# Kernel tuning notes

Measured on AMD Instinct MI355X. Metric: run time of the kernel, lower is better.

Reference implementation:

```python
import jax, jax.numpy as jnp
import numpy as np

B, S, D = 4, 1024, 2048
H, KVH, HD = 32, 8, 64
N_REP = H // KVH  # 4
ROPE_THETA = 1000000.0


def _rope_tables(seq_len, head_dim, theta):
    inv_freq = 1.0 / (theta ** (np.arange(0, head_dim, 2, dtype=np.float32) / head_dim))
    t = np.arange(seq_len, dtype=np.float32)
    freqs = np.outer(t, inv_freq)                      # (S, HD/2)
    emb = np.concatenate([freqs, freqs], axis=-1)      # (S, HD)
    return jnp.asarray(np.cos(emb)), jnp.asarray(np.sin(emb))


def setup_inputs() -> dict:
    key = jax.random.key(0)
    kx, kq, kk, kv, ko = jax.random.split(key, 5)
    cos, sin = _rope_tables(S, HD, ROPE_THETA)
    s = 0.02
    return {
        "x": jax.random.normal(kx, (B, S, D), jnp.float32),
        "cos": cos,
        "sin": sin,
        "Wq": jax.random.normal(kq, (D, H * HD), jnp.float32) * s,
        "Wk": jax.random.normal(kk, (D, KVH * HD), jnp.float32) * s,
        "Wv": jax.random.normal(kv, (D, KVH * HD), jnp.float32) * s,
        "Wo": jax.random.normal(ko, (H * HD, D), jnp.float32) * s,
    }


def _rotate_half(t):
    t1, t2 = jnp.split(t, 2, axis=-1)
    return jnp.concatenate([-t2, t1], axis=-1)


def reference(x, cos, sin, Wq, Wk, Wv, Wo):
    # projections
    q = (x @ Wq).reshape(B, S, H, HD)      # (b, s, h, d)
    k = (x @ Wk).reshape(B, S, KVH, HD)
    v = (x @ Wv).reshape(B, S, KVH, HD)

    # RoPE: cos/sin (s, d) broadcast over heads (unsqueeze_dim=1 -> (s,1,d))
    c = cos[:, None, :]
    sn = sin[:, None, :]
    q = q * c + _rotate_half(q) * sn
    k = k * c + _rotate_half(k) * sn

    # GQA attention without physically repeating KV:
    # q grouped as (b, kvh, n_rep, s, d); repeat_kv '(h r)' maps q head g*n_rep+r -> kv head g
    qg = q.transpose(0, 2, 1, 3).reshape(B, KVH, N_REP, S, HD)
    kt = k.transpose(0, 2, 1, 3)  # (b, kvh, s, d)
    vt = v.transpose(0, 2, 1, 3)

    scale = 1.0 / jnp.sqrt(jnp.asarray(HD, x.dtype))
    scores = jnp.einsum('bgrqd,bgkd->bgrqk', qg, kt) * scale  # (b, kvh, rep, s, s)
    probs = jax.nn.softmax(scores, axis=-1)
    out = jnp.einsum('bgrqk,bgkd->bgrqd', probs, vt)           # (b, kvh, rep, s, d)

    out = out.reshape(B, H, S, HD).transpose(0, 2, 1, 3).reshape(B, S, H * HD)
    return out @ Wo
```

## Files before the change

### kernel.cpp

```cpp
#include <hip/hip_runtime.h>

typedef unsigned short u16;
typedef __attribute__((ext_vector_type(8))) __bf16 bf16x8;
typedef __attribute__((ext_vector_type(4))) _Float16 f16x4;
typedef __attribute__((ext_vector_type(8))) _Float16 f16x8;
typedef __attribute__((ext_vector_type(4))) float f32x4;

#define BB 4
#define SS 1024
#define DD 2048
#define HH 32
#define KVHN 8
#define HDIM 64

__device__ __forceinline__ u16 f2b(float f) {
    union { float f; unsigned u; } v; v.f = f;
    unsigned r = v.u + 0x7FFFu + ((v.u >> 16) & 1u);
    return (u16)(r >> 16);
}
__device__ __forceinline__ float b2f(u16 h) {
    union { unsigned u; float f; } v; v.u = ((unsigned)h) << 16; return v.f;
}

__device__ __forceinline__ f32x4 mfma16(bf16x8 a, bf16x8 b, f32x4 c) {
    return __builtin_amdgcn_mfma_f32_16x16x32_bf16(a, b, c, 0, 0, 0);
}
__device__ __forceinline__ f32x4 mfma16h(f16x8 a, f16x8 b, f32x4 c) {
    return __builtin_amdgcn_mfma_f32_16x16x32_f16(a, b, c, 0, 0, 0);
}

__device__ __forceinline__ void async_cp16(const void* g, void* l) {
    __builtin_amdgcn_global_load_lds((__attribute__((address_space(1))) void*)g,
                                     (__attribute__((address_space(3))) void*)l,
                                     16, 0, 0);
}

__device__ __forceinline__ void block_sync() {
    asm volatile("" ::: "memory");
    __builtin_amdgcn_s_barrier();
    asm volatile("" ::: "memory");
}

__device__ __forceinline__ f16x8 pack8_f16(const float* p) {
    union { unsigned u[4]; f16x8 v; } pu;
    pu.u[0] = __builtin_bit_cast(unsigned, __builtin_amdgcn_cvt_pkrtz(p[0], p[1]));
    pu.u[1] = __builtin_bit_cast(unsigned, __builtin_amdgcn_cvt_pkrtz(p[2], p[3]));
    pu.u[2] = __builtin_bit_cast(unsigned, __builtin_amdgcn_cvt_pkrtz(p[4], p[5]));
    pu.u[3] = __builtin_bit_cast(unsigned, __builtin_amdgcn_cvt_pkrtz(p[6], p[7]));
    return pu.v;
}

__global__ __launch_bounds__(256) void cast_x_kernel(const float* __restrict__ x,
                                                     u16* __restrict__ xb) {
    int i = (blockIdx.x * 256 + threadIdx.x) * 4;
    float4 v = *(const float4*)(x + i);
    unsigned r0 = (unsigned)f2b(v.x) | ((unsigned)f2b(v.y) << 16);
    unsigned r1 = (unsigned)f2b(v.z) | ((unsigned)f2b(v.w) << 16);
    *(uint2*)(xb + i) = make_uint2(r0, r1);
}

__global__ __launch_bounds__(256) void wtrans_all_kernel(const float* __restrict__ Wq,
                                                         const float* __restrict__ Wk,
                                                         const float* __restrict__ Wv,
                                                         const float* __restrict__ Wo,
                                                         u16* __restrict__ Wqkvt,
                                                         u16* __restrict__ Wot) {
    __shared__ float tile[32][33];
    int z = blockIdx.z;
    const float* W = (z == 0) ? Wq : (z == 1) ? Wk : (z == 2) ? Wv : Wo;
    int N = (z == 1 || z == 2) ? 512 : 2048;
    int n_off = (z == 1) ? 2048 : (z == 2) ? 2560 : 0;
    u16* Wt = (z == 3) ? Wot : Wqkvt;
    int n0 = blockIdx.x * 32;
    if (n0 >= N) return;
    int k0 = blockIdx.y * 32;
    int tid = threadIdx.x;
    int nj = tid & 31;
    int ki = tid >> 5;
#pragma unroll
    for (int it = 0; it < 4; it++) {
        int kk = it * 8 + ki;
        tile[kk][nj] = W[(size_t)(k0 + kk) * N + n0 + nj];
    }
    __syncthreads();
#pragma unroll
    for (int it = 0; it < 4; it++) {
        int nn = it * 8 + ki;
        Wt[(size_t)(n0 + nn + n_off) * 2048 + k0 + nj] = f2b(tile[nj][nn]);
    }
}

__global__ __launch_bounds__(512, 2) void gemm_qkv(const u16* __restrict__ A,
                                                   const u16* __restrict__ Bt,
                                                   u16* __restrict__ C) {
    __shared__ __align__(16) u16 Ls[2][32768];
    const int tid = threadIdx.x;
    const int lane = tid & 63;
    const int w = tid >> 6;

    const int bid = blockIdx.x;
    const int xcd = bid & 7;
    const int loc = bid >> 3;
    const int mt = (xcd & 3) * 4 + (loc & 3);
    const int nt = (xcd >> 2) * 6 + (loc >> 2);
    const int m0 = mt * 256;
    const int n0 = nt * 256;

    const int wm = (w >> 2) * 128;
    const int wn = (w & 3) * 64;
    const int lr = lane & 15;
    const int lg = lane >> 4;

    const int row0 = tid >> 2;
    const int g = tid & 3;
    const int sg = g ^ ((row0 >> 1) & 3);
    const u16* pA0 = A + (size_t)(m0 + row0) * 2048 + sg * 8;
    const u16* pA1 = pA0 + (size_t)128 * 2048;
    const u16* pB0 = Bt + (size_t)(n0 + row0) * 2048 + sg * 8;
    const u16* pB1 = pB0 + (size_t)128 * 2048;

#define QSTA(buf_, ks_, T_)                                                     \
    {                                                                           \
        async_cp16(pA0 + (T_) * 64 + (ks_) * 32, &Ls[buf_][(ks_) * 8192 + w * 512]);        \
        async_cp16(pA1 + (T_) * 64 + (ks_) * 32, &Ls[buf_][(ks_) * 8192 + 4096 + w * 512]); \
    }
#define QSTB(buf_, ks_, T_)                                                     \
    {                                                                           \
        async_cp16(pB0 + (T_) * 64 + (ks_) * 32, &Ls[buf_][16384 + (ks_) * 8192 + w * 512]);        \
        async_cp16(pB1 + (T_) * 64 + (ks_) * 32, &Ls[buf_][16384 + (ks_) * 8192 + 4096 + w * 512]); \
    }

    f32x4 acc[8][4];
    const f32x4 zero4 = {0.f, 0.f, 0.f, 0.f};
#pragma unroll
    for (int i = 0; i < 8; i++)
#pragma unroll
        for (int j = 0; j < 4; j++) acc[i][j] = zero4;

    bf16x8 af[8], bfr[4];

#define QLDA(ks_)                                                               \
    _Pragma("unroll") for (int mi = 0; mi < 8; mi++) {                          \
        int r_ = wm + mi * 16 + lr;                                             \
        af[mi] = *(const bf16x8*)(&Ls[cur][(ks_) * 8192 + r_ * 32 + ((lg ^ ((r_ >> 1) & 3)) * 8)]); \
    }
#define QLDB(ks_, nb_)                                                          \
    _Pragma("unroll") for (int q_ = 0; q_ < 2; q_++) {                          \
        int ni_ = (nb_) * 2 + q_;                                               \
        int r_ = wn + ni_ * 16 + lr;                                            \
        bfr[ni_] = *(const bf16x8*)(&Ls[cur][16384 + (ks_) * 8192 + r_ * 32 + ((lg ^ ((r_ >> 1) & 3)) * 8)]); \
    }
#define QMM(nb_)                                                                \
    __builtin_amdgcn_s_setprio(1);                                              \
    _Pragma("unroll") for (int mi = 0; mi < 8; mi++) _Pragma("unroll") for (int q_ = 0; q_ < 2; q_++) { \
        int ni_ = (nb_) * 2 + q_;                                               \
        acc[mi][ni_] = mfma16(af[mi], bfr[ni_], acc[mi][ni_]);                  \
    }                                                                           \
    __builtin_amdgcn_s_setprio(0);
#define QWAITMM                                                                 \
    asm volatile("s_waitcnt lgkmcnt(0)" ::: "memory");                          \
    __builtin_amdgcn_sched_barrier(0);

    QSTA(0, 0, 0); QSTB(0, 0, 0); QSTA(0, 1, 0); QSTB(0, 1, 0);
    QSTA(1, 0, 1); QSTB(1, 0, 1);
    asm volatile("s_waitcnt vmcnt(4)" ::: "memory");
    block_sync();

#pragma unroll 2
    for (int T = 0; T < 32; ++T) {
        const int cur = T & 1;
        const int oth = cur ^ 1;
        const int Tp1 = (T + 1) & 31;
        const int Tp2 = (T + 2) & 31;

        QLDA(0); QLDB(0, 0);
        QSTA(oth, 1, Tp1);
        block_sync(); QWAITMM;
        QMM(0);
        block_sync();
        QLDB(0, 1);
        QSTB(oth, 1, Tp1);
        block_sync(); QWAITMM;
        QMM(1);
        block_sync();
        QLDA(1); QLDB(1, 0);
        QSTA(cur, 0, Tp2);
        block_sync(); QWAITMM;
        QMM(0);
        block_sync();
        QLDB(1, 1);
        QSTB(cur, 0, Tp2);
        block_sync(); QWAITMM;
        QMM(1);
        asm volatile("s_waitcnt vmcnt(4)" ::: "memory");
        block_sync();
    }
    asm volatile("s_waitcnt vmcnt(0)" ::: "memory");

    const int lq = lg * 4;
#pragma unroll
    for (int mi = 0; mi < 8; mi++)
#pragma unroll
        for (int ni = 0; ni < 4; ni++)
#pragma unroll
            for (int i = 0; i < 4; i++) {
                int r = m0 + wm + mi * 16 + lq + i;
                int c = n0 + wn + ni * 16 + lr;
                C[(size_t)r * 3072 + c] = f2b(acc[mi][ni][i]);
            }
#undef QSTA
#undef QSTB
#undef QLDA
#undef QLDB
#undef QMM
#undef QWAITMM
}

__global__ __launch_bounds__(512, 2) void gemm_out(const u16* __restrict__ A,
                                                   const u16* __restrict__ Bt,
                                                   float* __restrict__ C) {
    __shared__ __align__(16) u16 Ls[2][24576];
    const int tid = threadIdx.x;
    const int lane = tid & 63;
    const int w = tid >> 6;

    const int bid = blockIdx.x;
    const int xcd = bid & 7;
    const int loc = bid >> 3;
    const int mt = (xcd & 3) * 4 + (loc & 3);
    const int nt = (xcd >> 2) * 8 + (loc >> 2);
    const int m0 = mt * 256;
    const int n0 = nt * 128;

    const int wm = (w >> 2) * 128;
    const int wn = (w & 3) * 32;
    const int lr = lane & 15;
    const int lg = lane >> 4;

    const int row0 = tid >> 2;
    const int g = tid & 3;
    const int sg = g ^ ((row0 >> 1) & 3);
    const u16* pA0 = A + (size_t)(m0 + row0) * 2048 + sg * 8;
    const u16* pA1 = pA0 + (size_t)128 * 2048;
    const u16* pB0 = Bt + (size_t)(n0 + row0) * 2048 + sg * 8;

#define OSTA(buf_, ks_, T_)                                                     \
    {                                                                           \
        async_cp16(pA0 + (T_) * 64 + (ks_) * 32, &Ls[buf_][(ks_) * 8192 + w * 512]);        \
        async_cp16(pA1 + (T_) * 64 + (ks_) * 32, &Ls[buf_][(ks_) * 8192 + 4096 + w * 512]); \
    }
#define OSTB(buf_, ks_, T_)                                                     \
    {                                                                           \
        async_cp16(pB0 + (T_) * 64 + (ks_) * 32, &Ls[buf_][16384 + (ks_) * 4096 + w * 512]); \
    }

    f32x4 acc[8][2];
    const f32x4 zero4 = {0.f, 0.f, 0.f, 0.f};
#pragma unroll
    for (int i = 0; i < 8; i++)
#pragma unroll
        for (int j = 0; j < 2; j++) acc[i][j] = zero4;

    bf16x8 af[8], bfr[2];

#define OLDA(ks_)                                                               \
    _Pragma("unroll") for (int mi = 0; mi < 8; mi++) {                          \
        int r_ = wm + mi * 16 + lr;                                             \
        af[mi] = *(const bf16x8*)(&Ls[cur][(ks_) * 8192 + r_ * 32 + ((lg ^ ((r_ >> 1) & 3)) * 8)]); \
    }
#define OLDB(ks_)                                                               \
    _Pragma("unroll") for (int ni = 0; ni < 2; ni++) {                          \
        int r_ = wn + ni * 16 + lr;                                             \
        bfr[ni] = *(const bf16x8*)(&Ls[cur][16384 + (ks_) * 4096 + r_ * 32 + ((lg ^ ((r_ >> 1) & 3)) * 8)]); \
    }
#define OMM                                                                     \
    __builtin_amdgcn_s_setprio(1);                                              \
    _Pragma("unroll") for (int mi = 0; mi < 8; mi++) _Pragma("unroll") for (int ni = 0; ni < 2; ni++) { \
        acc[mi][ni] = mfma16(af[mi], bfr[ni], acc[mi][ni]);                     \
    }                                                                           \
    __builtin_amdgcn_s_setprio(0);
#define OWAITMM                                                                 \
    asm volatile("s_waitcnt lgkmcnt(0)" ::: "memory");                          \
    __builtin_amdgcn_sched_barrier(0);

    OSTA(0, 0, 0); OSTB(0, 0, 0); OSTA(0, 1, 0); OSTB(0, 1, 0);
    OSTA(1, 0, 1); OSTB(1, 0, 1);
    asm volatile("s_waitcnt vmcnt(3)" ::: "memory");
    block_sync();

#pragma unroll 2
    for (int T = 0; T < 32; ++T) {
        const int cur = T & 1;
        const int oth = cur ^ 1;
        const int Tp1 = (T + 1) & 31;
        const int Tp2 = (T + 2) & 31;

        OLDA(0); OLDB(0);
        OSTA(oth, 1, Tp1); OSTB(oth, 1, Tp1);
        block_sync(); OWAITMM;
        OMM;
        block_sync();
        OLDA(1); OLDB(1);
        OSTA(cur, 0, Tp2); OSTB(cur, 0, Tp2);
        block_sync(); OWAITMM;
        OMM;
        asm volatile("s_waitcnt vmcnt(3)" ::: "memory");
        block_sync();
    }
    asm volatile("s_waitcnt vmcnt(0)" ::: "memory");

    const int lq = lg * 4;
#pragma unroll
    for (int mi = 0; mi < 8; mi++)
#pragma unroll
        for (int ni = 0; ni < 2; ni++)
#pragma unroll
            for (int i = 0; i < 4; i++) {
                int r = m0 + wm + mi * 16 + lq + i;
                int c = n0 + wn + ni * 16 + lr;
                C[(size_t)r * 2048 + c] = acc[mi][ni][i];
            }
#undef OSTA
#undef OSTB
#undef OLDA
#undef OLDB
#undef OMM
#undef OWAITMM
}

__global__ __launch_bounds__(256) void rope_kernel(const u16* __restrict__ QKV,
                                                   const float* __restrict__ cosT,
                                                   const float* __restrict__ sinT,
                                                   u16* __restrict__ Qh,
                                                   u16* __restrict__ Kh) {
    const float QSC = 0.125f * 1.44269504088896f;
    int idx = blockIdx.x * 256 + threadIdx.x;
    int d = idx & 31;
    int t = idx >> 5;
    int hh = t % 40;
    int row = t / 40;
    int s = row & (SS - 1);
    int b = row >> 10;
    float c = cosT[s * HDIM + d];
    float sn = sinT[s * HDIM + d];
    if (hh < 32) {
        const u16* src = QKV + (size_t)row * 3072 + hh * 64 + d;
        float x1 = b2f(src[0]), x2 = b2f(src[32]);
        u16* dst = Qh + ((size_t)(b * HH + hh) * SS + s) * 64 + d;
        dst[0] = f2b((x1 * c - x2 * sn) * QSC);
        dst[32] = f2b((x2 * c + x1 * sn) * QSC);
    } else {
        int g = hh - 32;
        const u16* src = QKV + (size_t)row * 3072 + 2048 + g * 64 + d;
        float x1 = b2f(src[0]), x2 = b2f(src[32]);
        int rr = s & 7;
        int kpos = (s & ~31) + ((rr >= 4) ? 16 : 0) + ((s >> 3) & 3) * 4 + (rr & 3);
        u16* dst = Kh + ((size_t)(b * KVHN + g) * SS + kpos) * 64 + d;
        dst[0] = f2b(x1 * c - x2 * sn);
        dst[32] = f2b(x2 * c + x1 * sn);
    }
}

__global__ __launch_bounds__(256) void vtrans_kernel(const u16* __restrict__ QKV,
                                                     u16* __restrict__ Vt) {
    __shared__ u16 tile[64][65];
    int blk = blockIdx.x;
    int st = blk & 15;
    int t2 = blk >> 4;
    int g = t2 & 7;
    int b = t2 >> 3;
    int tid = threadIdx.x;
    int cj = tid & 63;
    int ri = tid >> 6;
    const u16* src = QKV + ((size_t)(b * SS + st * 64)) * 3072 + 2560 + g * 64;
#pragma unroll
    for (int it = 0; it < 16; it++) {
        int s_i = it * 4 + ri;
        tile[s_i][cj] = src[(size_t)s_i * 3072 + cj];
    }
    __syncthreads();
    u16* dst = Vt + ((size_t)(b * KVHN + g) * HDIM) * SS + st * 64;
#pragma unroll
    for (int it = 0; it < 16; it++) {
        int hd_i = it * 4 + ri;
        _Float16 hv = (_Float16)b2f(tile[cj][hd_i]);
        union { _Float16 h; u16 u; } cv; cv.h = hv;
        dst[(size_t)hd_i * SS + cj] = cv.u;
    }
}

__global__ __launch_bounds__(256, 4) void flash_kernel(const u16* __restrict__ Qh,
                                                       const u16* __restrict__ Kh,
                                                       const u16* __restrict__ Vt,
                                                       u16* __restrict__ Attn) {
    __shared__ __align__(16) u16 Kls[2][4096];
    __shared__ __align__(16) u16 Vls[2][4096];
    const int tid = threadIdx.x;
    const int lane = tid & 63;
    const int w = tid >> 6;
    const int bid = blockIdx.x;
    const int gbp = ((bid & 7) << 2) | ((bid >> 3) & 3);
    const int qt = bid >> 5;
    const int g = gbp & 7;
    const int b = gbp >> 3;
    const int h = g * 4 + w;
    const int lr = lane & 15;
    const int lg = lane >> 4;
    const int lk8 = lg * 8;
    const int lq = lg * 4;

    const u16* Qbase = Qh + ((size_t)(b * HH + h) * SS + qt * 32) * HDIM;
    bf16x8 qb[2][2];
#pragma unroll
    for (int j = 0; j < 2; j++) {
        qb[j][0] = *(const bf16x8*)(Qbase + (size_t)(j * 16 + lr) * HDIM + lk8);
        qb[j][1] = *(const bf16x8*)(Qbase + (size_t)(j * 16 + lr) * HDIM + 32 + lk8);
    }

    const u16* Kbase = Kh + (size_t)(b * KVHN + g) * SS * HDIM;
    const u16* Vbase = Vt + (size_t)(b * KVHN + g) * HDIM * SS;

    const int r0 = tid >> 3;
    const int c0 = tid & 7;

    const f32x4 zero4 = {0.f, 0.f, 0.f, 0.f};
    const f32x4 initS = {-4.f, -4.f, -4.f, -4.f};
    f32x4 o[2][4];
    float lsum[2] = {0.f, 0.f};
#pragma unroll
    for (int j = 0; j < 2; j++)
#pragma unroll
        for (int i = 0; i < 4; i++) o[j][i] = zero4;

#define STAGE(kt, p)                                                              \
    {                                                                             \
        _Pragma("unroll") for (int sh = 0; sh < 2; sh++) {                        \
            int rr = r0 + sh * 32;                                                \
            int cs = c0 ^ (rr & 7);                                              \
            async_cp16(Kbase + (size_t)((kt) + rr) * HDIM + cs * 8,               \
                       &Kls[p][sh * 2048 + w * 512]);                             \
            async_cp16(Vbase + (size_t)rr * SS + (kt) + cs * 8,                   \
                       &Vls[p][sh * 2048 + w * 512]);                             \
        }                                                                         \
    }

    STAGE(0, 0);
    __syncthreads();

    for (int t = 0; t < 16; t++) {
        const int p = t & 1;
        if (t < 15) STAGE((t + 1) * 64, p ^ 1);

#pragma unroll
        for (int c = 0; c < 2; c++) {
            f32x4 s[2][2];
#pragma unroll
            for (int halfi = 0; halfi < 2; halfi++) {
                const int R = c * 32 + halfi * 16 + lr;
                const u16* kr = &Kls[p][R * 64];
                bf16x8 kb0 = *(const bf16x8*)(kr + ((lg ^ (R & 7)) * 8));
                bf16x8 kb1 = *(const bf16x8*)(kr + (((4 + lg) ^ (R & 7)) * 8));
#pragma unroll
                for (int j = 0; j < 2; j++) {
                    f32x4 a = initS;
                    a = mfma16(kb0, qb[j][0], a);
                    a = mfma16(kb1, qb[j][1], a);
                    s[halfi][j] = a;
                }
            }

            f16x8 va[4];
#pragma unroll
            for (int hdt = 0; hdt < 4; hdt++) {
                const int R2 = hdt * 16 + lr;
                va[hdt] = *(const f16x8*)(&Vls[p][R2 * 64 + (((c * 4 + lg) ^ (R2 & 7)) * 8)]);
            }

#pragma unroll
            for (int j = 0; j < 2; j++) {
                float pv[8];
#pragma unroll
                for (int r = 0; r < 4; r++) {
                    pv[r] = __builtin_amdgcn_exp2f(s[0][j][r]);
                    pv[4 + r] = __builtin_amdgcn_exp2f(s[1][j][r]);
                }
                lsum[j] += ((pv[0] + pv[1]) + (pv[2] + pv[3])) +
                           ((pv[4] + pv[5]) + (pv[6] + pv[7]));
                f16x8 pb = pack8_f16(pv);
#pragma unroll
                for (int hdt = 0; hdt < 4; hdt++)
                    o[j][hdt] = mfma16h(va[hdt], pb, o[j][hdt]);
            }
        }
        __syncthreads();
    }

#pragma unroll
    for (int j = 0; j < 2; j++) {
        float su = lsum[j];
        su += __shfl_xor(su, 16);
        su += __shfl_xor(su, 32);
        float inv = 1.f / su;
        u16* Ob = Attn + ((size_t)(b * SS + qt * 32 + j * 16 + lr)) * 2048 + h * 64;
#pragma unroll
        for (int hdt = 0; hdt < 4; hdt++) {
            unsigned r0p = (unsigned)f2b(o[j][hdt][0] * inv) | ((unsigned)f2b(o[j][hdt][1] * inv) << 16);
            unsigned r1p = (unsigned)f2b(o[j][hdt][2] * inv) | ((unsigned)f2b(o[j][hdt][3] * inv) << 16);
            *(uint2*)(Ob + hdt * 16 + lq) = make_uint2(r0p, r1p);
        }
    }
}

extern "C" void kernel_launch(void* const* d_in, const int* in_sizes, int n_in,
                              void* d_out, int out_size, void* d_ws, size_t ws_size,
                              hipStream_t stream) {
    (void)in_sizes; (void)n_in; (void)out_size; (void)ws_size;
    const float* x = (const float*)d_in[0];
    const float* cosT = (const float*)d_in[1];
    const float* sinT = (const float*)d_in[2];
    const float* Wq = (const float*)d_in[3];
    const float* Wk = (const float*)d_in[4];
    const float* Wv = (const float*)d_in[5];
    const float* Wo = (const float*)d_in[6];
    float* out = (float*)d_out;

    char* ws = (char*)d_ws;
    u16* Xb    = (u16*)(ws);
    u16* Wqkvt = (u16*)(ws + 16777216);
    u16* Wot   = (u16*)(ws + 29360128);
    u16* QKV   = (u16*)(ws + 37748736);
    u16* Qh    = (u16*)(ws + 62914560);
    u16* Kh    = (u16*)(ws + 79691776);
    u16* Vt    = (u16*)(ws + 83886080);
    u16* Attn  = (u16*)(ws + 88080384);

    cast_x_kernel<<<8192, 256, 0, stream>>>(x, Xb);
    wtrans_all_kernel<<<dim3(64, 64, 4), 256, 0, stream>>>(Wq, Wk, Wv, Wo, Wqkvt, Wot);

    gemm_qkv<<<192, 512, 0, stream>>>(Xb, Wqkvt, QKV);

    rope_kernel<<<20480, 256, 0, stream>>>(QKV, cosT, sinT, Qh, Kh);
    vtrans_kernel<<<512, 256, 0, stream>>>(QKV, Vt);

    flash_kernel<<<1024, 256, 0, stream>>>(Qh, Kh, Vt, Attn);

    gemm_out<<<256, 512, 0, stream>>>(Attn, Wot, out);
}
```

Before: 270.5 us.

## Restructure QKV GEMM shared-memory layout and ping-pong load schedule

Rewrites the QKV projection GEMM's staging so each row holds a full 64-wide K slice with an 8-way XOR swizzle. The main loop now splits the 256x256 tile into M/N halves that are loaded and multiplied in a staggered order, with A and B tiles refilled into alternate buffers. The intent is to improve overlap of async global-to-LDS copies with MFMA work and to cut LDS bank conflicts and per-iteration barriers. The staggered buffer reuse makes the correctness of the wait counts and barrier placement delicate.

Measured after the change: 272.2 us. About the same (+0.6%).

```diff
diff --git a/kernel.cpp b/kernel.cpp
--- a/kernel.cpp
+++ b/kernel.cpp
@@ -106,28 +106,25 @@
     const int m0 = mt * 256;
     const int n0 = nt * 256;
 
-    const int wm = (w >> 2) * 128;
+    const int wm_h = w >> 2;
     const int wn = (w & 3) * 64;
     const int lr = lane & 15;
     const int lg = lane >> 4;
 
-    const int row0 = tid >> 2;
-    const int g = tid & 3;
-    const int sg = g ^ ((row0 >> 1) & 3);
-    const u16* pA0 = A + (size_t)(m0 + row0) * 2048 + sg * 8;
-    const u16* pA1 = pA0 + (size_t)128 * 2048;
-    const u16* pB0 = Bt + (size_t)(n0 + row0) * 2048 + sg * 8;
-    const u16* pB1 = pB0 + (size_t)128 * 2048;
-
-#define QSTA(buf_, ks_, T_)                                                     \
-    {                                                                           \
-        async_cp16(pA0 + (T_) * 64 + (ks_) * 32, &Ls[buf_][(ks_) * 8192 + w * 512]);        \
-        async_cp16(pA1 + (T_) * 64 + (ks_) * 32, &Ls[buf_][(ks_) * 8192 + 4096 + w * 512]); \
-    }
-#define QSTB(buf_, ks_, T_)                                                     \
-    {                                                                           \
-        async_cp16(pB0 + (T_) * 64 + (ks_) * 32, &Ls[buf_][16384 + (ks_) * 8192 + w * 512]);        \
-        async_cp16(pB1 + (T_) * 64 + (ks_) * 32, &Ls[buf_][16384 + (ks_) * 8192 + 4096 + w * 512]); \
+    const int sr = lane >> 3;
+    const int sl = (lane & 7) ^ (sr & 7);
+    const u16* pA = A + (size_t)(m0 + w * 8 + sr) * 2048 + sl * 8;
+    const u16* pB = Bt + (size_t)(n0 + w * 8 + sr) * 2048 + sl * 8;
+
+#define STA(buf_, h_, kt_)                                                               \
+    {                                                                                    \
+        async_cp16(pA + (size_t)((h_) * 128) * 2048 + (kt_) * 64, &Ls[buf_][(h_) * 8192 + w * 512]);            \
+        async_cp16(pA + (size_t)((h_) * 128 + 64) * 2048 + (kt_) * 64, &Ls[buf_][(h_) * 8192 + 4096 + w * 512]); \
+    }
+#define STB(buf_, h_, kt_)                                                               \
+    {                                                                                    \
+        async_cp16(pB + (size_t)((h_) * 128) * 2048 + (kt_) * 64, &Ls[buf_][16384 + (h_) * 8192 + w * 512]);            \
+        async_cp16(pB + (size_t)((h_) * 128 + 64) * 2048 + (kt_) * 64, &Ls[buf_][16384 + (h_) * 8192 + 4096 + w * 512]); \
     }
 
     f32x4 acc[8][4];
@@ -137,67 +134,86 @@
 #pragma unroll
         for (int j = 0; j < 4; j++) acc[i][j] = zero4;
 
-    bf16x8 af[8], bfr[4];
-
-#define QLDA(ks_)                                                               \
-    _Pragma("unroll") for (int mi = 0; mi < 8; mi++) {                          \
-        int r_ = wm + mi * 16 + lr;                                             \
-        af[mi] = *(const bf16x8*)(&Ls[cur][(ks_) * 8192 + r_ * 32 + ((lg ^ ((r_ >> 1) & 3)) * 8)]); \
-    }
-#define QLDB(ks_, nb_)                                                          \
-    _Pragma("unroll") for (int q_ = 0; q_ < 2; q_++) {                          \
-        int ni_ = (nb_) * 2 + q_;                                               \
-        int r_ = wn + ni_ * 16 + lr;                                            \
-        bfr[ni_] = *(const bf16x8*)(&Ls[cur][16384 + (ks_) * 8192 + r_ * 32 + ((lg ^ ((r_ >> 1) & 3)) * 8)]); \
-    }
-#define QMM(nb_)                                                                \
-    __builtin_amdgcn_s_setprio(1);                                              \
-    _Pragma("unroll") for (int mi = 0; mi < 8; mi++) _Pragma("unroll") for (int q_ = 0; q_ < 2; q_++) { \
-        int ni_ = (nb_) * 2 + q_;                                               \
-        acc[mi][ni_] = mfma16(af[mi], bfr[ni_], acc[mi][ni_]);                  \
-    }                                                                           \
+    bf16x8 af[8], b0[4], b1[4];
+
+#define LDA(mh_, buf_)                                                                   \
+    _Pragma("unroll") for (int mi = 0; mi < 4; mi++) _Pragma("unroll") for (int ks = 0; ks < 2; ks++) { \
+        int rh = (mh_) * 64 + mi * 16 + lr;                                              \
+        af[mi * 2 + ks] = *(const bf16x8*)(&Ls[buf_][wm_h * 8192 + rh * 64 + (((ks * 4 + lg) ^ (lr & 7)) * 8)]); \
+    }
+#define LDB(dst_, nh_, buf_)                                                             \
+    _Pragma("unroll") for (int ni = 0; ni < 2; ni++) _Pragma("unroll") for (int ks = 0; ks < 2; ks++) { \
+        int rowb = wn + (nh_) * 32 + ni * 16 + lr;                                       \
+        dst_[ni * 2 + ks] = *(const bf16x8*)(&Ls[buf_][16384 + (rowb >> 7) * 8192 + (rowb & 127) * 64 + (((ks * 4 + lg) ^ (lr & 7)) * 8)]); \
+    }
+#define QMM(mh_, nh_, bb_)                                                               \
+    __builtin_amdgcn_s_setprio(1);                                                       \
+    _Pragma("unroll") for (int mi = 0; mi < 4; mi++) _Pragma("unroll") for (int ni = 0; ni < 2; ni++) { \
+        acc[(mh_) * 4 + mi][(nh_) * 2 + ni] = mfma16(af[mi * 2 + 0], bb_[ni * 2 + 0], acc[(mh_) * 4 + mi][(nh_) * 2 + ni]); \
+        acc[(mh_) * 4 + mi][(nh_) * 2 + ni] = mfma16(af[mi * 2 + 1], bb_[ni * 2 + 1], acc[(mh_) * 4 + mi][(nh_) * 2 + ni]); \
+    }                                                                                    \
     __builtin_amdgcn_s_setprio(0);
-#define QWAITMM                                                                 \
-    asm volatile("s_waitcnt lgkmcnt(0)" ::: "memory");                          \
+#define WAITLDS                                                                          \
+    asm volatile("s_waitcnt lgkmcnt(0)" ::: "memory");                                   \
     __builtin_amdgcn_sched_barrier(0);
 
-    QSTA(0, 0, 0); QSTB(0, 0, 0); QSTA(0, 1, 0); QSTB(0, 1, 0);
-    QSTA(1, 0, 1); QSTB(1, 0, 1);
-    asm volatile("s_waitcnt vmcnt(4)" ::: "memory");
+    STA(0, 0, 0); STA(0, 1, 0); STB(0, 0, 0); STB(0, 1, 0);
+    STB(1, 0, 1); STB(1, 1, 1);
+    asm volatile("s_waitcnt vmcnt(0)" ::: "memory");
     block_sync();
 
-#pragma unroll 2
-    for (int T = 0; T < 32; ++T) {
-        const int cur = T & 1;
-        const int oth = cur ^ 1;
-        const int Tp1 = (T + 1) & 31;
-        const int Tp2 = (T + 2) & 31;
-
-        QLDA(0); QLDB(0, 0);
-        QSTA(oth, 1, Tp1);
-        block_sync(); QWAITMM;
-        QMM(0);
-        block_sync();
-        QLDB(0, 1);
-        QSTB(oth, 1, Tp1);
-        block_sync(); QWAITMM;
-        QMM(1);
-        block_sync();
-        QLDA(1); QLDB(1, 0);
-        QSTA(cur, 0, Tp2);
-        block_sync(); QWAITMM;
-        QMM(0);
-        block_sync();
-        QLDB(1, 1);
-        QSTB(cur, 0, Tp2);
-        block_sync(); QWAITMM;
-        QMM(1);
+#pragma unroll 1
+    for (int I = 0; I < 16; ++I) {
+        const int tb = 2 * I + 1;
+        const int ta2 = (2 * I + 2) & 31;
+        const int tb2 = (2 * I + 3) & 31;
+
+        LDA(0, 0); LDB(b0, 0, 0);
+        STA(1, 0, tb);
+        block_sync(); WAITLDS;
+        QMM(0, 0, b0);
+        block_sync();
+        LDB(b1, 1, 0);
+        STA(1, 1, tb);
+        block_sync(); WAITLDS;
+        QMM(0, 1, b1);
+        block_sync();
+        LDA(1, 0);
+        STB(0, 0, ta2);
+        block_sync(); WAITLDS;
+        QMM(1, 1, b1);
+        block_sync();
+        STB(0, 1, ta2);
+        block_sync(); WAITLDS;
+        QMM(1, 0, b0);
         asm volatile("s_waitcnt vmcnt(4)" ::: "memory");
         block_sync();
+
+        LDA(0, 1); LDB(b0, 0, 1);
+        STA(0, 0, ta2);
+        block_sync(); WAITLDS;
+        QMM(0, 0, b0);
+        block_sync();
+        LDB(b1, 1, 1);
+        STA(0, 1, ta2);
+        block_sync(); WAITLDS;
+        QMM(0, 1, b1);
+        block_sync();
+        LDA(1, 1);
+        STB(1, 0, tb2);
+        block_sync(); WAITLDS;
+        QMM(1, 1, b1);
+        block_sync();
+        STB(1, 1, tb2);
+        block_sync(); WAITLDS;
+        QMM(1, 0, b0);
+        asm volatile("s_waitcnt vmcnt(4)" ::: "memory");
+        block_sync();
     }
     asm volatile("s_waitcnt vmcnt(0)" ::: "memory");
 
     const int lq = lg * 4;
+    const int wm = wm_h * 128;
 #pragma unroll
     for (int mi = 0; mi < 8; mi++)
 #pragma unroll
@@ -208,12 +224,12 @@
                 int c = n0 + wn + ni * 16 + lr;
                 C[(size_t)r * 3072 + c] = f2b(acc[mi][ni][i]);
             }
-#undef QSTA
-#undef QSTB
-#undef QLDA
-#undef QLDB
+#undef STA
+#undef STB
+#undef LDA
+#undef LDB
 #undef QMM
-#undef QWAITMM
+#undef WAITLDS
 }
 
 __global__ __launch_bounds__(512, 2) void gemm_out(const u16* __restrict__ A,
```
